# Optimization experiments

Measured on AMD Instinct MI355X. Metric: run time of the kernel, lower is better.

## Reference

```python
import jax, jax.numpy as jnp
import numpy as np

T, B, I, H = 512, 64, 1024, 1024
DROPOUT = 0.3


def setup_inputs() -> dict:
    key = jax.random.key(0)
    k = jax.random.split(key, 6)
    s = 1.0 / np.sqrt(H).astype(np.float32)
    x = jax.random.normal(k[0], (T, B, I), dtype=jnp.float32)
    w_ih = jax.random.uniform(k[1], (4 * H, I), minval=-s, maxval=s, dtype=jnp.float32)
    w_hh = jax.random.uniform(k[2], (4 * H, H), minval=-s, maxval=s, dtype=jnp.float32)
    b_ih = jax.random.uniform(k[3], (4 * H,), minval=-s, maxval=s, dtype=jnp.float32)
    b_hh = jax.random.uniform(k[4], (4 * H,), minval=-s, maxval=s, dtype=jnp.float32)
    # init_weights: forget-gate bias (second quarter) set to 1
    b_ih = b_ih.at[H:2 * H].set(1.0)
    b_hh = b_hh.at[H:2 * H].set(1.0)
    # DropConnect mask on recurrent weights (training-mode dropout, fixed realization)
    keep = jax.random.bernoulli(k[5], 1.0 - DROPOUT, (4 * H, H))
    hh_mask = keep.astype(jnp.float32) / (1.0 - DROPOUT)
    return {"x": x, "w_ih": w_ih, "w_hh": w_hh, "b_ih": b_ih, "b_hh": b_hh, "hh_mask": hh_mask}


def reference(x, w_ih, w_hh, b_ih, b_hh, hh_mask):
    # x: (T, B, I). PyTorch LSTM gate order: i, f, g, o.
    h = w_hh.shape[1]
    w_hh_dropped = w_hh * hh_mask  # DropConnect applied once per forward
    # Precompute input contribution for all timesteps (one big GEMM): (T, B, 4H)
    gx = jnp.einsum('tbi,gi->tbg', x, w_ih) + b_ih + b_hh

    def step(carry, g_t):
        h_t, c_t = carry
        gates = g_t + h_t @ w_hh_dropped.T  # (B, 4H)
        i_g, f_g, g_g, o_g = jnp.split(gates, 4, axis=-1)
        i_g = jax.nn.sigmoid(i_g)
        f_g = jax.nn.sigmoid(f_g)
        g_g = jnp.tanh(g_g)
        o_g = jax.nn.sigmoid(o_g)
        c_new = f_g * c_t + i_g * g_g
        h_new = o_g * jnp.tanh(c_new)
        return (h_new, c_new), h_new

    bsz = x.shape[1]
    init = (jnp.zeros((bsz, h), x.dtype), jnp.zeros((bsz, h), x.dtype))
    (hn, cn), out = jax.lax.scan(step, init, gx)
    # match torch: output (T,B,H), hn/cn with leading num_layers dim
    return out, hn[None], cn[None]
```

## Files before the change

### kernel.cpp

```cpp
#include <hip/hip_runtime.h>

#define TT 512
#define BB 64
#define II 1024
#define HH 1024
#define GG 4096
#define BH 65536
#define NBLK 128

typedef __attribute__((ext_vector_type(8))) short bf16x8;
typedef __attribute__((ext_vector_type(4))) float f32x4;
typedef __attribute__((ext_vector_type(4))) unsigned u32x4;

__device__ __forceinline__ float bf2f(unsigned short u) {
  union { unsigned int i; float f; } v; v.i = ((unsigned int)u) << 16; return v.f;
}
__device__ __forceinline__ unsigned short f2bf(float f) {
  union { float f; unsigned int i; } v; v.f = f;
  return (unsigned short)((v.i + 0x7FFFu + ((v.i >> 16) & 1u)) >> 16);
}
__device__ __forceinline__ bf16x8 pack8(float4 a, float4 b) {
  union { bf16x8 v; unsigned short u[8]; } p;
  p.u[0] = f2bf(a.x); p.u[1] = f2bf(a.y); p.u[2] = f2bf(a.z); p.u[3] = f2bf(a.w);
  p.u[4] = f2bf(b.x); p.u[5] = f2bf(b.y); p.u[6] = f2bf(b.z); p.u[7] = f2bf(b.w);
  return p.v;
}
__device__ __forceinline__ float sigmoid_f(float x) { return 1.0f / (1.0f + __expf(-x)); }
__device__ __forceinline__ float tanh_f(float x) {
  float e = __expf(-2.0f * fabsf(x));
  float t = (1.0f - e) / (1.0f + e);
  return copysignf(t, x);
}

__device__ __forceinline__ void st32_uc(unsigned* p, unsigned v) {
  __hip_atomic_store(p, v, __ATOMIC_RELAXED, __HIP_MEMORY_SCOPE_AGENT);
}
__device__ __forceinline__ unsigned ld32_uc(const unsigned* p) {
  return __hip_atomic_load(p, __ATOMIC_RELAXED, __HIP_MEMORY_SCOPE_AGENT);
}
__device__ __forceinline__ void st128_uc(void* p, u32x4 v) {
  asm volatile("global_store_dwordx4 %0, %1, off sc0 sc1" :: "v"(p), "v"(v) : "memory");
}
__device__ __forceinline__ void lds_add_rel(int* p) {
  __hip_atomic_fetch_add(p, 1, __ATOMIC_RELEASE, __HIP_MEMORY_SCOPE_WORKGROUP);
}
__device__ __forceinline__ int lds_ld_acq(const int* p) {
  return __hip_atomic_load(p, __ATOMIC_ACQUIRE, __HIP_MEMORY_SCOPE_WORKGROUP);
}
__device__ __forceinline__ void lds_st_rel(int* p, int v) {
  __hip_atomic_store(p, v, __ATOMIC_RELEASE, __HIP_MEMORY_SCOPE_WORKGROUP);
}

__global__ __launch_bounds__(256) void wdlstm_xconv(
    const float* __restrict__ xc, unsigned short* __restrict__ xbf, int n4) {
  int stride = gridDim.x * blockDim.x;
  for (int i = blockIdx.x * blockDim.x + threadIdx.x; i < n4; i += stride) {
    float4 v = *(const float4*)(xc + (size_t)i * 4);
    unsigned short o[4] = {f2bf(v.x), f2bf(v.y), f2bf(v.z), f2bf(v.w)};
    *(unsigned long long*)(xbf + (size_t)i * 4) = *(unsigned long long*)o;
  }
}

__global__ __launch_bounds__(576) void wdlstm_fused(
    const float* __restrict__ w_hh, const float* __restrict__ hh_mask,
    const float* __restrict__ w_ih,
    const float* __restrict__ b_ih, const float* __restrict__ b_hh,
    const unsigned short* __restrict__ xbf,
    float* __restrict__ out, float* __restrict__ c_state,
    unsigned* __restrict__ flags,
    unsigned short* __restrict__ hinit,
    unsigned short* __restrict__ hring,
    int t0, int tc) {
  __shared__ __align__(16) char Wh[65536];
  __shared__ __align__(16) char Wi[65536];
  __shared__ float Dlds[64][33];
  __shared__ __align__(8) unsigned short Dgx[4][32][72];
  __shared__ __align__(16) unsigned Hs[64][4];
  __shared__ int syncv[8];

  const int tid = threadIdx.x;
  const int wv  = tid >> 6, l = tid & 63;
  const int ln  = l & 15, lq = l >> 4;
  const int j0h = blockIdx.x * 8;
  unsigned* g_step = flags + 2048;

  for (int c = tid; c < 4096; c += 576) {
    int n = c >> 7, cc = c & 127;
    int wrow = (n >> 3) * HH + j0h + (n & 7);
    int addr = (n * 2048 + cc * 16) ^ ((n & 7) << 4);
    {
      const float* sw = w_hh   + (size_t)wrow * HH + cc * 8;
      const float* sm = hh_mask + (size_t)wrow * HH + cc * 8;
      float4 w0 = *(const float4*)sw, w1 = *(const float4*)(sw + 4);
      float4 m0 = *(const float4*)sm, m1 = *(const float4*)(sm + 4);
      float4 p0 = {w0.x * m0.x, w0.y * m0.y, w0.z * m0.z, w0.w * m0.w};
      float4 p1 = {w1.x * m1.x, w1.y * m1.y, w1.z * m1.z, w1.w * m1.w};
      *(bf16x8*)(Wh + addr) = pack8(p0, p1);
    }
    {
      const float* si = w_ih + (size_t)wrow * II + cc * 8;
      float4 a0 = *(const float4*)si, a1 = *(const float4*)(si + 4);
      *(bf16x8*)(Wi + addr) = pack8(a0, a1);
    }
  }
  if (tid < 8) syncv[tid] = 0;
  __syncthreads();

  if (wv < 4) {
    const int b_ep = l;
    const int jj0  = 2 * wv;
    float c_reg[2];
    if (t0 == 0) { c_reg[0] = c_reg[1] = 0.f; }
    else {
      float2 cv = *(const float2*)(c_state + (size_t)b_ep * HH + j0h + jj0);
      c_reg[0] = cv.x; c_reg[1] = cv.y;
    }
    float biasv[4][2];
#pragma unroll
    for (int g = 0; g < 4; ++g)
#pragma unroll
      for (int q = 0; q < 2; ++q) {
        int col = g * HH + j0h + jj0 + q;
        biasv[g][q] = b_ih[col] + b_hh[col];
      }
    float* hn_out = out + (size_t)TT * BH;
    float* cn_out = hn_out + BH;

    for (int lt = 0; lt < tc; ++lt) {
      const int t = t0 + lt;
      f32x4 acc[2];
      acc[0] = (f32x4){0.f, 0.f, 0.f, 0.f};
      acc[1] = (f32x4){0.f, 0.f, 0.f, 0.f};

      if (t > 0) {
        while ((int)ld32_uc(g_step) < t) __builtin_amdgcn_s_sleep(1);
        const unsigned short* hp = (lt == 0) ? hinit : hring + (size_t)(lt - 1) * BH;
        const unsigned short* ap = hp + (size_t)(16 * wv + ln) * HH + lq * 8;
        bf16x8 aA[8], aB[8];
#pragma unroll
        for (int i = 0; i < 8; ++i) aA[i] = *(const bf16x8*)(ap + i * 32);
#pragma unroll
        for (int c4 = 0; c4 < 4; ++c4) {
          const bf16x8* cur = (c4 & 1) ? aB : aA;
          bf16x8*       nxt = (c4 & 1) ? aA : aB;
          if (c4 < 3) {
#pragma unroll
            for (int i = 0; i < 8; ++i) nxt[i] = *(const bf16x8*)(ap + (c4 + 1) * 256 + i * 32);
          }
#pragma unroll
          for (int i = 0; i < 8; ++i) {
            int kc = c4 * 8 + i;
#pragma unroll
            for (int ni = 0; ni < 2; ++ni) {
              int n = 16 * ni + ln;
              int baddr = (n * 2048 + kc * 64 + lq * 16) ^ ((n & 7) << 4);
              bf16x8 b = *(const bf16x8*)(Wh + baddr);
              acc[ni] = __builtin_amdgcn_mfma_f32_16x16x32_bf16(cur[i], b, acc[ni], 0, 0, 0);
            }
          }
        }
      }
#pragma unroll
      for (int ni = 0; ni < 2; ++ni)
#pragma unroll
        for (int r = 0; r < 4; ++r)
          Dlds[16 * wv + 4 * lq + r][16 * ni + ln] = acc[ni][r];
      if (l == 0) lds_add_rel(&syncv[0]);
      {
        const int tgt = 4 * (lt + 1);
        while (lds_ld_acq(&syncv[0]) < tgt) __builtin_amdgcn_s_sleep(1);
        while (lds_ld_acq(&syncv[2]) < lt + 1 || lds_ld_acq(&syncv[3]) < lt + 1 ||
               lds_ld_acq(&syncv[4]) < lt + 1 || lds_ld_acq(&syncv[5]) < lt + 1)
          __builtin_amdgcn_s_sleep(1);
      }

      const int slot = lt & 3;
      float hq[2];
#pragma unroll
      for (int q = 0; q < 2; ++q) {
        int jj = jj0 + q;
        float g0 = Dlds[b_ep][ 0 + jj] + bf2f(Dgx[slot][ 0 + jj][b_ep]) + biasv[0][q];
        float g1 = Dlds[b_ep][ 8 + jj] + bf2f(Dgx[slot][ 8 + jj][b_ep]) + biasv[1][q];
        float g2 = Dlds[b_ep][16 + jj] + bf2f(Dgx[slot][16 + jj][b_ep]) + biasv[2][q];
        float g3 = Dlds[b_ep][24 + jj] + bf2f(Dgx[slot][24 + jj][b_ep]) + biasv[3][q];
        float ig = sigmoid_f(g0);
        float fg = sigmoid_f(g1);
        float gg = tanh_f(g2);
        float og = sigmoid_f(g3);
        c_reg[q] = fg * c_reg[q] + ig * gg;
        hq[q] = og * tanh_f(c_reg[q]);
      }
      *(float2*)(out + (size_t)t * BH + (size_t)b_ep * HH + j0h + jj0) = make_float2(hq[0], hq[1]);
      Hs[b_ep][wv] = (unsigned)f2bf(hq[0]) | ((unsigned)f2bf(hq[1]) << 16);
      if (t == TT - 1) {
        *(float2*)(hn_out + (size_t)b_ep * HH + j0h + jj0) = make_float2(hq[0], hq[1]);
        *(float2*)(cn_out + (size_t)b_ep * HH + j0h + jj0) = make_float2(c_reg[0], c_reg[1]);
      }
      if (l == 0) lds_add_rel(&syncv[1]);

      if (wv == 0) {
        const int tgt = 4 * (lt + 1);
        while (lds_ld_acq(&syncv[1]) < tgt) __builtin_amdgcn_s_sleep(1);
        u32x4 hv4 = *(const u32x4*)&Hs[l][0];
        char* dst = (char*)hring + ((size_t)lt * BH + (size_t)l * HH + j0h) * 2;
        st128_uc(dst, hv4);
        if (lt == tc - 1) {
          char* dsti = (char*)hinit + ((size_t)l * HH + j0h) * 2;
          st128_uc(dsti, hv4);
        }
        asm volatile("s_waitcnt vmcnt(0)" ::: "memory");
        if (l == 0) st32_uc(&flags[blockIdx.x * 16], (unsigned)(t + 1));
      }
    }
    *(float2*)(c_state + (size_t)b_ep * HH + j0h + jj0) = make_float2(c_reg[0], c_reg[1]);

  } else if (wv < 8) {
    const int w2 = wv - 4;
    for (int s = 0; s < tc; ++s) {
      if (s >= 4) {
        const int tgt = 4 * (s - 3);
        while (lds_ld_acq(&syncv[1]) < tgt) __builtin_amdgcn_s_sleep(1);
      }
      f32x4 acc[2];
      acc[0] = (f32x4){0.f, 0.f, 0.f, 0.f};
      acc[1] = (f32x4){0.f, 0.f, 0.f, 0.f};
      const unsigned short* ap = xbf + (size_t)s * BH + (size_t)(16 * w2 + ln) * II + lq * 8;
      bf16x8 aA[8], aB[8];
#pragma unroll
      for (int i = 0; i < 8; ++i) aA[i] = *(const bf16x8*)(ap + i * 32);
#pragma unroll
      for (int c4 = 0; c4 < 4; ++c4) {
        const bf16x8* cur = (c4 & 1) ? aB : aA;
        bf16x8*       nxt = (c4 & 1) ? aA : aB;
        if (c4 < 3) {
#pragma unroll
          for (int i = 0; i < 8; ++i) nxt[i] = *(const bf16x8*)(ap + (c4 + 1) * 256 + i * 32);
        }
#pragma unroll
        for (int i = 0; i < 8; ++i) {
          int kc = c4 * 8 + i;
#pragma unroll
          for (int ni = 0; ni < 2; ++ni) {
            int n = 16 * ni + ln;
            int baddr = (n * 2048 + kc * 64 + lq * 16) ^ ((n & 7) << 4);
            bf16x8 b = *(const bf16x8*)(Wi + baddr);
            acc[ni] = __builtin_amdgcn_mfma_f32_16x16x32_bf16(cur[i], b, acc[ni], 0, 0, 0);
          }
        }
      }
      const int slot = s & 3;
#pragma unroll
      for (int ni = 0; ni < 2; ++ni) {
        unsigned short p[4] = {f2bf(acc[ni][0]), f2bf(acc[ni][1]),
                               f2bf(acc[ni][2]), f2bf(acc[ni][3])};
        *(unsigned long long*)&Dgx[slot][16 * ni + ln][16 * w2 + 4 * lq] =
            *(unsigned long long*)p;
      }
      if (l == 0) lds_st_rel(&syncv[2 + w2], s + 1);
    }

  } else if (blockIdx.x == 0) {
    const unsigned* f0 = flags + (2 * l) * 16;
    const unsigned* f1 = flags + (2 * l + 1) * 16;
    for (int s = t0; s < t0 + tc; ++s) {
      while ((int)ld32_uc(f0) < s || (int)ld32_uc(f1) < s)
        __builtin_amdgcn_s_sleep(1);
      if (l == 0) st32_uc(g_step, (unsigned)s);
    }
  }
}

extern "C" void kernel_launch(void* const* d_in, const int* in_sizes, int n_in,
                              void* d_out, int out_size, void* d_ws, size_t ws_size,
                              hipStream_t stream) {
  const float* x       = (const float*)d_in[0];
  const float* w_ih    = (const float*)d_in[1];
  const float* w_hh    = (const float*)d_in[2];
  const float* b_ih    = (const float*)d_in[3];
  const float* b_hh    = (const float*)d_in[4];
  const float* hh_mask = (const float*)d_in[5];
  float* out           = (float*)d_out;

  char* ws = (char*)d_ws;
  float* c_state        = (float*)ws;
  unsigned* flags       = (unsigned*)(ws + 262144);
  unsigned short* hinit = (unsigned short*)(ws + 278528);
  unsigned short* hring = (unsigned short*)(ws + 409600);

  const long long fixed = 409600;
  const long long per_t = 131072 + 131072;
  long long avail = (long long)ws_size - fixed;
  int TC = (int)(avail / per_t);
  if (TC > 128) TC = 128;
  if (TC < 2) TC = 2;
  unsigned short* xbf = (unsigned short*)(ws + 409600 + (size_t)TC * 131072);

  hipMemsetAsync(flags, 0, 16384, stream);

  for (int t0 = 0; t0 < TT; t0 += TC) {
    int tc = TT - t0 < TC ? TT - t0 : TC;
    const float* xc = x + (size_t)t0 * BB * II;
    wdlstm_xconv<<<256, 256, 0, stream>>>(xc, xbf, tc * BH / 4);
    wdlstm_fused<<<NBLK, 576, 0, stream>>>(w_hh, hh_mask, w_ih, b_ih, b_hh, xbf,
                                           out, c_state, flags, hinit, hring, t0, tc);
  }
}
```

Measured before the change: 4.824 ms.

## Publish per-K-chunk progress so recurrent GEMM starts on partially ready hidden state

The global step barrier becomes a progress counter. The coordinator now publishes how many of eight K-groups of the previous hidden state are complete, using a ballot over per-block flags. Consumer waves wait only for the K-chunk they need next and load A fragments in groups of four, so the recurrent MFMA work can overlap with blocks that are still finishing the previous step. The cost is more frequent polling of the global counter and a shallower prefetch depth.

```diff
diff --git a/kernel.cpp b/kernel.cpp
--- a/kernel.cpp
+++ b/kernel.cpp
@@ -82,7 +82,7 @@
   const int wv  = tid >> 6, l = tid & 63;
   const int ln  = l & 15, lq = l >> 4;
   const int j0h = blockIdx.x * 8;
-  unsigned* g_step = flags + 2048;
+  unsigned* g_prog = flags + 2048;
 
   for (int c = tid; c < 4096; c += 576) {
     int n = c >> 7, cc = c & 127;
@@ -133,23 +133,33 @@
       acc[1] = (f32x4){0.f, 0.f, 0.f, 0.f};
 
       if (t > 0) {
-        while ((int)ld32_uc(g_step) < t) __builtin_amdgcn_s_sleep(1);
         const unsigned short* hp = (lt == 0) ? hinit : hring + (size_t)(lt - 1) * BH;
         const unsigned short* ap = hp + (size_t)(16 * wv + ln) * HH + lq * 8;
-        bf16x8 aA[8], aB[8];
-#pragma unroll
-        for (int i = 0; i < 8; ++i) aA[i] = *(const bf16x8*)(ap + i * 32);
-#pragma unroll
-        for (int c4 = 0; c4 < 4; ++c4) {
-          const bf16x8* cur = (c4 & 1) ? aB : aA;
-          bf16x8*       nxt = (c4 & 1) ? aA : aB;
-          if (c4 < 3) {
-#pragma unroll
-            for (int i = 0; i < 8; ++i) nxt[i] = *(const bf16x8*)(ap + (c4 + 1) * 256 + i * 32);
+        int avail = (lt == 0) ? 8 : 0;
+        auto ensure = [&](int g) {
+          while (avail <= g) {
+            int v = (int)ld32_uc(g_prog) - 8 * t;
+            if (v > 8) v = 8;
+            if (v > avail) avail = v; else __builtin_amdgcn_s_sleep(1);
           }
-#pragma unroll
-          for (int i = 0; i < 8; ++i) {
-            int kc = c4 * 8 + i;
+        };
+        bf16x8 a0[4], a1[4];
+        ensure(0);
+#pragma unroll
+        for (int i = 0; i < 4; ++i) a0[i] = *(const bf16x8*)(ap + i * 32);
+#pragma unroll
+        for (int g = 0; g < 8; ++g) {
+          bf16x8* cur = (g & 1) ? a1 : a0;
+          bf16x8* nxt = (g & 1) ? a0 : a1;
+          if (g < 7) {
+            ensure(g + 1);
+#pragma unroll
+            for (int i = 0; i < 4; ++i)
+              nxt[i] = *(const bf16x8*)(ap + (4 * (g + 1) + i) * 32);
+          }
+#pragma unroll
+          for (int i = 0; i < 4; ++i) {
+            int kc = 4 * g + i;
 #pragma unroll
             for (int ni = 0; ni < 2; ++ni) {
               int n = 16 * ni + ln;
@@ -262,10 +272,20 @@
   } else if (blockIdx.x == 0) {
     const unsigned* f0 = flags + (2 * l) * 16;
     const unsigned* f1 = flags + (2 * l + 1) * 16;
-    for (int s = t0; s < t0 + tc; ++s) {
-      while ((int)ld32_uc(f0) < s || (int)ld32_uc(f1) < s)
-        __builtin_amdgcn_s_sleep(1);
-      if (l == 0) st32_uc(g_step, (unsigned)s);
+    for (int s = t0 + 1; s < t0 + tc; ++s) {
+      int pub = 0;
+      while (pub < 8) {
+        bool mine = ((int)ld32_uc(f0) >= s) && ((int)ld32_uc(f1) >= s);
+        unsigned long long b = __ballot(mine);
+        int ng = 0;
+        while (ng < 8 && ((b >> (8 * ng)) & 0xFFull) == 0xFFull) ++ng;
+        if (ng > pub) {
+          pub = ng;
+          if (l == 0) st32_uc(g_prog, (unsigned)(8 * s + ng));
+        } else {
+          __builtin_amdgcn_s_sleep(1);
+        }
+      }
     }
   }
 }
```

Result: faster. 4.518 ms (-6.3%).

## Replace flag-based grid barrier with sentinel polling on the h ring buffer

Applied to the files above, without the earlier changes.

Removes the global step flags and the coordinator wave that gathered per-block flags into a global step counter. The ring buffer is now pre-filled with 0xFFFF sentinels, and each consumer wave polls its own h fragments until they no longer hold a sentinel before feeding them to MFMA. This takes a two-hop flag round trip and a store-completion wait off the per-step critical path. In exchange it adds a memset per chunk and assumes no real bf16 h value equals 0xFFFF (a NaN pattern). It also lifts the time-chunk cap up to the full sequence, so fewer launches may be needed.

```diff
diff --git a/kernel.cpp b/kernel.cpp
--- a/kernel.cpp
+++ b/kernel.cpp
@@ -32,14 +32,22 @@
   return copysignf(t, x);
 }
 
-__device__ __forceinline__ void st32_uc(unsigned* p, unsigned v) {
-  __hip_atomic_store(p, v, __ATOMIC_RELAXED, __HIP_MEMORY_SCOPE_AGENT);
-}
-__device__ __forceinline__ unsigned ld32_uc(const unsigned* p) {
-  return __hip_atomic_load(p, __ATOMIC_RELAXED, __HIP_MEMORY_SCOPE_AGENT);
-}
 __device__ __forceinline__ void st128_uc(void* p, u32x4 v) {
   asm volatile("global_store_dwordx4 %0, %1, off sc0 sc1" :: "v"(p), "v"(v) : "memory");
+}
+__device__ __forceinline__ u32x4 ld128_uc(const void* p) {
+  u32x4 v;
+  asm volatile("global_load_dwordx4 %0, %1, off sc0 sc1\n\ts_waitcnt vmcnt(0)"
+               : "=v"(v) : "v"(p) : "memory");
+  return v;
+}
+__device__ __forceinline__ bool frag_ok(u32x4 w) {
+#pragma unroll
+  for (int i = 0; i < 4; ++i) {
+    unsigned x = w[i];
+    if ((x & 0xFFFFu) == 0xFFFFu || (x >> 16) == 0xFFFFu) return false;
+  }
+  return true;
 }
 __device__ __forceinline__ void lds_add_rel(int* p) {
   __hip_atomic_fetch_add(p, 1, __ATOMIC_RELEASE, __HIP_MEMORY_SCOPE_WORKGROUP);
@@ -61,13 +69,12 @@
   }
 }
 
-__global__ __launch_bounds__(576) void wdlstm_fused(
+__global__ __launch_bounds__(512) void wdlstm_fused(
     const float* __restrict__ w_hh, const float* __restrict__ hh_mask,
     const float* __restrict__ w_ih,
     const float* __restrict__ b_ih, const float* __restrict__ b_hh,
     const unsigned short* __restrict__ xbf,
     float* __restrict__ out, float* __restrict__ c_state,
-    unsigned* __restrict__ flags,
     unsigned short* __restrict__ hinit,
     unsigned short* __restrict__ hring,
     int t0, int tc) {
@@ -82,9 +89,8 @@
   const int wv  = tid >> 6, l = tid & 63;
   const int ln  = l & 15, lq = l >> 4;
   const int j0h = blockIdx.x * 8;
-  unsigned* g_step = flags + 2048;
-
-  for (int c = tid; c < 4096; c += 576) {
+
+  for (int c = tid; c < 4096; c += 512) {
     int n = c >> 7, cc = c & 127;
     int wrow = (n >> 3) * HH + j0h + (n & 7);
     int addr = (n * 2048 + cc * 16) ^ ((n & 7) << 4);
@@ -133,29 +139,40 @@
       acc[1] = (f32x4){0.f, 0.f, 0.f, 0.f};
 
       if (t > 0) {
-        while ((int)ld32_uc(g_step) < t) __builtin_amdgcn_s_sleep(1);
-        const unsigned short* hp = (lt == 0) ? hinit : hring + (size_t)(lt - 1) * BH;
-        const unsigned short* ap = hp + (size_t)(16 * wv + ln) * HH + lq * 8;
-        bf16x8 aA[8], aB[8];
-#pragma unroll
-        for (int i = 0; i < 8; ++i) aA[i] = *(const bf16x8*)(ap + i * 32);
-#pragma unroll
-        for (int c4 = 0; c4 < 4; ++c4) {
-          const bf16x8* cur = (c4 & 1) ? aB : aA;
-          bf16x8*       nxt = (c4 & 1) ? aA : aB;
-          if (c4 < 3) {
-#pragma unroll
-            for (int i = 0; i < 8; ++i) nxt[i] = *(const bf16x8*)(ap + (c4 + 1) * 256 + i * 32);
+        const bool poll = (lt != 0);
+        const char* ap = (const char*)((lt == 0) ? hinit : hring + (size_t)(lt - 1) * BH)
+                         + (size_t)(16 * wv + ln) * 2048 + lq * 16;
+        u32x4 p0[4], p1[4];
+#pragma unroll
+        for (int i = 0; i < 4; ++i) p0[i] = *(const u32x4*)(ap + i * 64);
+#pragma unroll
+        for (int g = 0; g < 8; ++g) {
+          u32x4* cur = (g & 1) ? p1 : p0;
+          u32x4* nxt = (g & 1) ? p0 : p1;
+          if (g < 7) {
+#pragma unroll
+            for (int i = 0; i < 4; ++i)
+              nxt[i] = *(const u32x4*)(ap + (4 * (g + 1) + i) * 64);
           }
-#pragma unroll
-          for (int i = 0; i < 8; ++i) {
-            int kc = c4 * 8 + i;
+          if (poll) {
+#pragma unroll
+            for (int i = 0; i < 4; ++i) {
+              while (!frag_ok(cur[i])) {
+                __builtin_amdgcn_s_sleep(1);
+                cur[i] = ld128_uc(ap + (4 * g + i) * 64);
+              }
+            }
+          }
+#pragma unroll
+          for (int i = 0; i < 4; ++i) {
+            int kc = 4 * g + i;
+            union { u32x4 w; bf16x8 a; } ua; ua.w = cur[i];
 #pragma unroll
             for (int ni = 0; ni < 2; ++ni) {
               int n = 16 * ni + ln;
               int baddr = (n * 2048 + kc * 64 + lq * 16) ^ ((n & 7) << 4);
               bf16x8 b = *(const bf16x8*)(Wh + baddr);
-              acc[ni] = __builtin_amdgcn_mfma_f32_16x16x32_bf16(cur[i], b, acc[ni], 0, 0, 0);
+              acc[ni] = __builtin_amdgcn_mfma_f32_16x16x32_bf16(ua.a, b, acc[ni], 0, 0, 0);
             }
           }
         }
@@ -205,16 +222,13 @@
         char* dst = (char*)hring + ((size_t)lt * BH + (size_t)l * HH + j0h) * 2;
         st128_uc(dst, hv4);
         if (lt == tc - 1) {
-          char* dsti = (char*)hinit + ((size_t)l * HH + j0h) * 2;
-          st128_uc(dsti, hv4);
+          *(u32x4*)((char*)hinit + ((size_t)l * HH + j0h) * 2) = hv4;
         }
-        asm volatile("s_waitcnt vmcnt(0)" ::: "memory");
-        if (l == 0) st32_uc(&flags[blockIdx.x * 16], (unsigned)(t + 1));
       }
     }
     *(float2*)(c_state + (size_t)b_ep * HH + j0h + jj0) = make_float2(c_reg[0], c_reg[1]);
 
-  } else if (wv < 8) {
+  } else {
     const int w2 = wv - 4;
     for (int s = 0; s < tc; ++s) {
       if (s >= 4) {
@@ -257,15 +271,6 @@
             *(unsigned long long*)p;
       }
       if (l == 0) lds_st_rel(&syncv[2 + w2], s + 1);
-    }
-
-  } else if (blockIdx.x == 0) {
-    const unsigned* f0 = flags + (2 * l) * 16;
-    const unsigned* f1 = flags + (2 * l + 1) * 16;
-    for (int s = t0; s < t0 + tc; ++s) {
-      while ((int)ld32_uc(f0) < s || (int)ld32_uc(f1) < s)
-        __builtin_amdgcn_s_sleep(1);
-      if (l == 0) st32_uc(g_step, (unsigned)s);
     }
   }
 }
@@ -283,25 +288,23 @@
 
   char* ws = (char*)d_ws;
   float* c_state        = (float*)ws;
-  unsigned* flags       = (unsigned*)(ws + 262144);
-  unsigned short* hinit = (unsigned short*)(ws + 278528);
-  unsigned short* hring = (unsigned short*)(ws + 409600);
-
-  const long long fixed = 409600;
+  unsigned short* hinit = (unsigned short*)(ws + 262144);
+  unsigned short* hring = (unsigned short*)(ws + 393216);
+
+  const long long fixed = 393216;
   const long long per_t = 131072 + 131072;
   long long avail = (long long)ws_size - fixed;
   int TC = (int)(avail / per_t);
-  if (TC > 128) TC = 128;
+  if (TC > TT) TC = TT;
   if (TC < 2) TC = 2;
-  unsigned short* xbf = (unsigned short*)(ws + 409600 + (size_t)TC * 131072);
-
-  hipMemsetAsync(flags, 0, 16384, stream);
+  unsigned short* xbf = (unsigned short*)(ws + 393216 + (size_t)TC * 131072);
 
   for (int t0 = 0; t0 < TT; t0 += TC) {
     int tc = TT - t0 < TC ? TT - t0 : TC;
     const float* xc = x + (size_t)t0 * BB * II;
     wdlstm_xconv<<<256, 256, 0, stream>>>(xc, xbf, tc * BH / 4);
-    wdlstm_fused<<<NBLK, 576, 0, stream>>>(w_hh, hh_mask, w_ih, b_ih, b_hh, xbf,
-                                           out, c_state, flags, hinit, hring, t0, tc);
-  }
-}
+    hipMemsetAsync(hring, 0xFF, (size_t)tc * 131072, stream);
+    wdlstm_fused<<<NBLK, 512, 0, stream>>>(w_hh, hh_mask, w_ih, b_ih, b_hh, xbf,
+                                           out, c_state, hinit, hring, t0, tc);
+  }
+}
```

New measurement: 6.817 ms. 1.41x slower.

## Replace central coordinator with per-block flag polling and per-wave epilogue

Applied to the files above, without the earlier changes.

Removes the dedicated coordinator wave in block 0 that aggregated all block flags into a global step counter. Each block's wave 0 now polls all 128 block flags directly and broadcasts readiness through LDS. The epilogue is restructured so each wave processes its own 16 batch rows without a cross-wave LDS barrier, and each wave writes its own slice of h to the ring. The chunk cap is raised so the time loop can run in fewer launches. This trades one global hop of latency per step for more polling traffic on the flag array from every block.

```diff
diff --git a/kernel.cpp b/kernel.cpp
--- a/kernel.cpp
+++ b/kernel.cpp
@@ -61,7 +61,7 @@
   }
 }
 
-__global__ __launch_bounds__(576) void wdlstm_fused(
+__global__ __launch_bounds__(512) void wdlstm_fused(
     const float* __restrict__ w_hh, const float* __restrict__ hh_mask,
     const float* __restrict__ w_ih,
     const float* __restrict__ b_ih, const float* __restrict__ b_hh,
@@ -73,18 +73,17 @@
     int t0, int tc) {
   __shared__ __align__(16) char Wh[65536];
   __shared__ __align__(16) char Wi[65536];
-  __shared__ float Dlds[64][33];
+  __shared__ float Dw[4][16][33];
   __shared__ __align__(8) unsigned short Dgx[4][32][72];
-  __shared__ __align__(16) unsigned Hs[64][4];
+  __shared__ __align__(16) unsigned Hsw[4][16][4];
   __shared__ int syncv[8];
 
   const int tid = threadIdx.x;
   const int wv  = tid >> 6, l = tid & 63;
   const int ln  = l & 15, lq = l >> 4;
   const int j0h = blockIdx.x * 8;
-  unsigned* g_step = flags + 2048;
-
-  for (int c = tid; c < 4096; c += 576) {
+
+  for (int c = tid; c < 4096; c += 512) {
     int n = c >> 7, cc = c & 127;
     int wrow = (n >> 3) * HH + j0h + (n & 7);
     int addr = (n * 2048 + cc * 16) ^ ((n & 7) << 4);
@@ -107,12 +106,12 @@
   __syncthreads();
 
   if (wv < 4) {
-    const int b_ep = l;
-    const int jj0  = 2 * wv;
+    const int b_ew = 16 * wv + ln;
+    const int jj0  = 2 * lq;
     float c_reg[2];
     if (t0 == 0) { c_reg[0] = c_reg[1] = 0.f; }
     else {
-      float2 cv = *(const float2*)(c_state + (size_t)b_ep * HH + j0h + jj0);
+      float2 cv = *(const float2*)(c_state + (size_t)b_ew * HH + j0h + jj0);
       c_reg[0] = cv.x; c_reg[1] = cv.y;
     }
     float biasv[4][2];
@@ -133,7 +132,17 @@
       acc[1] = (f32x4){0.f, 0.f, 0.f, 0.f};
 
       if (t > 0) {
-        while ((int)ld32_uc(g_step) < t) __builtin_amdgcn_s_sleep(1);
+        if (lt > 0) {
+          if (wv == 0) {
+            const unsigned* f0 = flags + (2 * l) * 16;
+            const unsigned* f1 = flags + (2 * l + 1) * 16;
+            while ((int)ld32_uc(f0) < t || (int)ld32_uc(f1) < t)
+              __builtin_amdgcn_s_sleep(1);
+            if (l == 0) lds_st_rel(&syncv[7], t);
+          } else {
+            while (lds_ld_acq(&syncv[7]) < t) {}
+          }
+        }
         const unsigned short* hp = (lt == 0) ? hinit : hring + (size_t)(lt - 1) * BH;
         const unsigned short* ap = hp + (size_t)(16 * wv + ln) * HH + lq * 8;
         bf16x8 aA[8], aB[8];
@@ -164,25 +173,22 @@
       for (int ni = 0; ni < 2; ++ni)
 #pragma unroll
         for (int r = 0; r < 4; ++r)
-          Dlds[16 * wv + 4 * lq + r][16 * ni + ln] = acc[ni][r];
-      if (l == 0) lds_add_rel(&syncv[0]);
-      {
-        const int tgt = 4 * (lt + 1);
-        while (lds_ld_acq(&syncv[0]) < tgt) __builtin_amdgcn_s_sleep(1);
-        while (lds_ld_acq(&syncv[2]) < lt + 1 || lds_ld_acq(&syncv[3]) < lt + 1 ||
-               lds_ld_acq(&syncv[4]) < lt + 1 || lds_ld_acq(&syncv[5]) < lt + 1)
-          __builtin_amdgcn_s_sleep(1);
-      }
+          Dw[wv][4 * lq + r][16 * ni + ln] = acc[ni][r];
+
+      while (lds_ld_acq(&syncv[2]) < lt + 1 || lds_ld_acq(&syncv[3]) < lt + 1 ||
+             lds_ld_acq(&syncv[4]) < lt + 1 || lds_ld_acq(&syncv[5]) < lt + 1)
+        __builtin_amdgcn_s_sleep(1);
+      asm volatile("s_waitcnt lgkmcnt(0)" ::: "memory");
 
       const int slot = lt & 3;
       float hq[2];
 #pragma unroll
       for (int q = 0; q < 2; ++q) {
         int jj = jj0 + q;
-        float g0 = Dlds[b_ep][ 0 + jj] + bf2f(Dgx[slot][ 0 + jj][b_ep]) + biasv[0][q];
-        float g1 = Dlds[b_ep][ 8 + jj] + bf2f(Dgx[slot][ 8 + jj][b_ep]) + biasv[1][q];
-        float g2 = Dlds[b_ep][16 + jj] + bf2f(Dgx[slot][16 + jj][b_ep]) + biasv[2][q];
-        float g3 = Dlds[b_ep][24 + jj] + bf2f(Dgx[slot][24 + jj][b_ep]) + biasv[3][q];
+        float g0 = Dw[wv][ln][ 0 + jj] + bf2f(Dgx[slot][ 0 + jj][b_ew]) + biasv[0][q];
+        float g1 = Dw[wv][ln][ 8 + jj] + bf2f(Dgx[slot][ 8 + jj][b_ew]) + biasv[1][q];
+        float g2 = Dw[wv][ln][16 + jj] + bf2f(Dgx[slot][16 + jj][b_ew]) + biasv[2][q];
+        float g3 = Dw[wv][ln][24 + jj] + bf2f(Dgx[slot][24 + jj][b_ew]) + biasv[3][q];
         float ig = sigmoid_f(g0);
         float fg = sigmoid_f(g1);
         float gg = tanh_f(g2);
@@ -190,31 +196,34 @@
         c_reg[q] = fg * c_reg[q] + ig * gg;
         hq[q] = og * tanh_f(c_reg[q]);
       }
-      *(float2*)(out + (size_t)t * BH + (size_t)b_ep * HH + j0h + jj0) = make_float2(hq[0], hq[1]);
-      Hs[b_ep][wv] = (unsigned)f2bf(hq[0]) | ((unsigned)f2bf(hq[1]) << 16);
+      if (l == 0) lds_add_rel(&syncv[1]);
+
+      *(float2*)(out + (size_t)t * BH + (size_t)b_ew * HH + j0h + jj0) = make_float2(hq[0], hq[1]);
+      Hsw[wv][ln][lq] = (unsigned)f2bf(hq[0]) | ((unsigned)f2bf(hq[1]) << 16);
       if (t == TT - 1) {
-        *(float2*)(hn_out + (size_t)b_ep * HH + j0h + jj0) = make_float2(hq[0], hq[1]);
-        *(float2*)(cn_out + (size_t)b_ep * HH + j0h + jj0) = make_float2(c_reg[0], c_reg[1]);
-      }
-      if (l == 0) lds_add_rel(&syncv[1]);
-
+        *(float2*)(hn_out + (size_t)b_ew * HH + j0h + jj0) = make_float2(hq[0], hq[1]);
+        *(float2*)(cn_out + (size_t)b_ew * HH + j0h + jj0) = make_float2(c_reg[0], c_reg[1]);
+      }
+      asm volatile("s_waitcnt lgkmcnt(0)" ::: "memory");
+
+      if (l < 16) {
+        u32x4 hv4 = *(const u32x4*)&Hsw[wv][l][0];
+        char* dst = (char*)hring + ((size_t)lt * BH + (size_t)(16 * wv + l) * HH + j0h) * 2;
+        st128_uc(dst, hv4);
+        if (lt == tc - 1)
+          *(u32x4*)((char*)hinit + ((size_t)(16 * wv + l) * HH + j0h) * 2) = hv4;
+      }
+      asm volatile("s_waitcnt vmcnt(0)" ::: "memory");
+      if (l == 0) lds_add_rel(&syncv[6]);
       if (wv == 0) {
         const int tgt = 4 * (lt + 1);
-        while (lds_ld_acq(&syncv[1]) < tgt) __builtin_amdgcn_s_sleep(1);
-        u32x4 hv4 = *(const u32x4*)&Hs[l][0];
-        char* dst = (char*)hring + ((size_t)lt * BH + (size_t)l * HH + j0h) * 2;
-        st128_uc(dst, hv4);
-        if (lt == tc - 1) {
-          char* dsti = (char*)hinit + ((size_t)l * HH + j0h) * 2;
-          st128_uc(dsti, hv4);
-        }
-        asm volatile("s_waitcnt vmcnt(0)" ::: "memory");
+        while (lds_ld_acq(&syncv[6]) < tgt) {}
         if (l == 0) st32_uc(&flags[blockIdx.x * 16], (unsigned)(t + 1));
       }
     }
-    *(float2*)(c_state + (size_t)b_ep * HH + j0h + jj0) = make_float2(c_reg[0], c_reg[1]);
-
-  } else if (wv < 8) {
+    *(float2*)(c_state + (size_t)b_ew * HH + j0h + jj0) = make_float2(c_reg[0], c_reg[1]);
+
+  } else {
     const int w2 = wv - 4;
     for (int s = 0; s < tc; ++s) {
       if (s >= 4) {
@@ -257,15 +266,6 @@
             *(unsigned long long*)p;
       }
       if (l == 0) lds_st_rel(&syncv[2 + w2], s + 1);
-    }
-
-  } else if (blockIdx.x == 0) {
-    const unsigned* f0 = flags + (2 * l) * 16;
-    const unsigned* f1 = flags + (2 * l + 1) * 16;
-    for (int s = t0; s < t0 + tc; ++s) {
-      while ((int)ld32_uc(f0) < s || (int)ld32_uc(f1) < s)
-        __builtin_amdgcn_s_sleep(1);
-      if (l == 0) st32_uc(g_step, (unsigned)s);
     }
   }
 }
@@ -284,24 +284,24 @@
   char* ws = (char*)d_ws;
   float* c_state        = (float*)ws;
   unsigned* flags       = (unsigned*)(ws + 262144);
-  unsigned short* hinit = (unsigned short*)(ws + 278528);
-  unsigned short* hring = (unsigned short*)(ws + 409600);
-
-  const long long fixed = 409600;
+  unsigned short* hinit = (unsigned short*)(ws + 270336);
+  unsigned short* hring = (unsigned short*)(ws + 401408);
+
+  const long long fixed = 401408;
   const long long per_t = 131072 + 131072;
   long long avail = (long long)ws_size - fixed;
   int TC = (int)(avail / per_t);
-  if (TC > 128) TC = 128;
+  if (TC > TT) TC = TT;
   if (TC < 2) TC = 2;
-  unsigned short* xbf = (unsigned short*)(ws + 409600 + (size_t)TC * 131072);
-
-  hipMemsetAsync(flags, 0, 16384, stream);
+  unsigned short* xbf = (unsigned short*)(ws + 401408 + (size_t)TC * 131072);
+
+  hipMemsetAsync(flags, 0, 8192, stream);
 
   for (int t0 = 0; t0 < TT; t0 += TC) {
     int tc = TT - t0 < TC ? TT - t0 : TC;
     const float* xc = x + (size_t)t0 * BB * II;
     wdlstm_xconv<<<256, 256, 0, stream>>>(xc, xbf, tc * BH / 4);
-    wdlstm_fused<<<NBLK, 576, 0, stream>>>(w_hh, hh_mask, w_ih, b_ih, b_hh, xbf,
+    wdlstm_fused<<<NBLK, 512, 0, stream>>>(w_hh, hh_mask, w_ih, b_ih, b_hh, xbf,
                                            out, c_state, flags, hinit, hring, t0, tc);
   }
 }
```

Result: faster. 4.640 ms (-3.8%).
